# Kernel optimization log

Measured on AMD Instinct MI355X. Metric: run time of the kernel, lower is better.

Reference implementation:

```python
import jax, jax.numpy as jnp
import numpy as np
from jax import lax

B, C, H, W = 16, 128, 128, 128
C8, C16 = C // 8, C // 16
LN_EPS = 1e-5


def dct_mat(N):
    # torch_dct.dct (norm=None): X_k = 2 * sum_n x_n cos(pi*(2n+1)k/(2N))
    n = jnp.arange(N, dtype=jnp.float32)
    k = jnp.arange(N, dtype=jnp.float32)
    return 2.0 * jnp.cos(jnp.pi * (2.0 * n[None, :] + 1.0) * k[:, None] / (2.0 * N))


def setup_inputs() -> dict:
    key = jax.random.key(0)
    ks = jax.random.split(key, 20)
    s = 0.05
    return {
        "x": jax.random.normal(ks[0], (B, C, H, W), dtype=jnp.float32),
        # channel attention (1x1 convs acting on GAP -> stored as dense [out,in])
        "ca_w1": jax.random.normal(ks[1], (C8, C), dtype=jnp.float32) * s,
        "ca_b1": jnp.zeros((C8,), jnp.float32),
        "ca_w2": jax.random.normal(ks[2], (C, C8), dtype=jnp.float32) * s,
        "ca_b2": jnp.zeros((C,), jnp.float32),
        # spatial attention 9x9 conv -> 1 channel
        "sa_w": jax.random.normal(ks[3], (1, C, 9, 9), dtype=jnp.float32) * s,
        "sa_b": jnp.zeros((1,), jnp.float32),
        # frequency channel attention MLP
        "fa_w1": jax.random.normal(ks[4], (C8, C), dtype=jnp.float32) * s,
        "fa_b1": jnp.zeros((C8,), jnp.float32),
        "fa_w2": jax.random.normal(ks[5], (C, C8), dtype=jnp.float32) * s,
        "fa_b2": jnp.zeros((C,), jnp.float32),
        # global context block
        "gc_mask_w": jax.random.normal(ks[6], (C,), dtype=jnp.float32) * s,
        "gc_mask_b": jnp.zeros((), jnp.float32),
        "gc_t1_w": jax.random.normal(ks[7], (C16, C), dtype=jnp.float32) * s,
        "gc_t1_b": jnp.zeros((C16,), jnp.float32),
        "gc_ln_g": jnp.ones((C16,), jnp.float32),
        "gc_ln_b": jnp.zeros((C16,), jnp.float32),
        "gc_t2_w": jax.random.normal(ks[8], (C, C16), dtype=jnp.float32) * s,
        "gc_t2_b": jnp.zeros((C,), jnp.float32),
        # branch mixing weights + output 1x1 conv
        "alpha": jnp.ones((4,), jnp.float32),
        "out_w": jax.random.normal(ks[9], (C, C), dtype=jnp.float32) * s,
        "out_b": jnp.zeros((C,), jnp.float32),
    }


def reference(x, ca_w1, ca_b1, ca_w2, ca_b2, sa_w, sa_b,
              fa_w1, fa_b1, fa_w2, fa_b2,
              gc_mask_w, gc_mask_b, gc_t1_w, gc_t1_b, gc_ln_g, gc_ln_b,
              gc_t2_w, gc_t2_b, alpha, out_w, out_b):
    b, c, h, w = x.shape
    # --- channel attention (SE-style) ---
    gap = x.mean(axis=(2, 3))                                   # [B,C]
    hca = jax.nn.relu(gap @ ca_w1.T + ca_b1)
    ca = jax.nn.sigmoid(hca @ ca_w2.T + ca_b2)                  # [B,C]
    ac = x * ca[:, :, None, None]
    # --- spatial attention (9x9 conv -> sigmoid gate) ---
    smap = lax.conv_general_dilated(x, sa_w, (1, 1), ((4, 4), (4, 4)),
                                    dimension_numbers=("NCHW", "OIHW", "NCHW"))
    as_ = jax.nn.sigmoid(smap + sa_b[None, :, None, None]) * x
    # --- frequency channel attention (DCT-II 2d, mean over freq) ---
    Dw = dct_mat(w)
    Dh = dct_mat(h)
    xf = jnp.einsum("bchw,kw->bchk", x, Dw)
    xf = jnp.einsum("bchk,lh->bclk", xf, Dh)                    # [B,C,H,W] freq
    favg = xf.mean(axis=(2, 3))                                 # [B,C]
    hfa = jax.nn.relu(favg @ fa_w1.T + fa_b1)
    fwt = jax.nn.sigmoid(hfa @ fa_w2.T + fa_b2)
    af = x * fwt[:, :, None, None]
    # --- global context block ---
    mask = jnp.einsum("bchw,c->bhw", x, gc_mask_w) + gc_mask_b  # [B,H,W]
    mask = jax.nn.softmax(mask.reshape(b, h * w), axis=-1)      # [B,HW]
    ctx = jnp.einsum("bcp,bp->bc", x.reshape(b, c, h * w), mask)  # [B,C]
    t = ctx @ gc_t1_w.T + gc_t1_b                               # [B,C/16]
    mu = t.mean(axis=-1, keepdims=True)
    var = ((t - mu) ** 2).mean(axis=-1, keepdims=True)
    t = (t - mu) * lax.rsqrt(var + LN_EPS) * gc_ln_g + gc_ln_b
    t = jax.nn.relu(t)
    ctx2 = t @ gc_t2_w.T + gc_t2_b                              # [B,C]
    ag = x + ctx2[:, :, None, None]
    # --- softmax-weighted fusion + output 1x1 conv ---
    wts = jax.nn.softmax(alpha)
    fused = wts[0] * ac + wts[1] * as_ + wts[2] * af + wts[3] * ag
    return jnp.einsum("bchw,oc->bohw", fused, out_w) + out_b[None, :, None, None]
```

## Files before the change

kernel.cpp:

```cpp
#include <hip/hip_runtime.h>
#include <math.h>

#define B_   16
#define C_   128
#define W_   128
#define HW_  16384

#define OFF_SARR 0
#define OFF_GAP  128
#define OFF_FAVG 2176
#define OFF_CTX  4224
#define OFF_G    6272
#define OFF_CB   8320
#define OFF_WTS  10368
#define OFF_PMAX 10496
#define OFF_PSUM 10752
#define OFF_SMX  11008
#define OFF_SINV 11024
#define OFF_WT   16384
#define OFF_M    32768
#define OFF_S    (32768 + 262144)
#define OFF_SMAP (32768 + 2 * 262144)

__device__ __forceinline__ float wave_reduce_sum(float v) {
#pragma unroll
  for (int o = 32; o > 0; o >>= 1) v += __shfl_down(v, o, 64);
  return v;
}

__global__ void k0_sarr(float* __restrict__ sarr) {
  int n = threadIdx.x;
  double a = 3.14159265358979323846 * (2.0 * n + 1.0) / 256.0;
  double v = 2.0 * sin(64.0 * a) * cos(63.5 * a) / sin(0.5 * a);
  sarr[n] = (float)v;
}

__global__ __launch_bounds__(256) void k1_planered(const float* __restrict__ x,
                                                   const float* __restrict__ sarr,
                                                   float* __restrict__ gap,
                                                   float* __restrict__ favg) {
  __shared__ float sL[128];
  __shared__ float buf[8];
  int tid = threadIdx.x;
  int bc = blockIdx.x;
  if (tid < 128) sL[tid] = sarr[tid];
  __syncthreads();
  const float* xp = x + (size_t)bc * HW_;
  float s0 = 0.f, s1 = 0.f;
  for (int i = tid << 2; i < HW_; i += 1024) {
    float4 v = *(const float4*)(xp + i);
    int y = i >> 7, xs = i & 127;
    float shy = sL[y];
    float d = v.x * sL[xs] + v.y * sL[xs + 1] + v.z * sL[xs + 2] + v.w * sL[xs + 3];
    s0 += v.x + v.y + v.z + v.w;
    s1 += shy * d;
  }
  s0 = wave_reduce_sum(s0);
  s1 = wave_reduce_sum(s1);
  int lane = tid & 63, wv = tid >> 6;
  if (lane == 0) { buf[wv] = s0; buf[4 + wv] = s1; }
  __syncthreads();
  if (tid == 0) {
    gap[bc]  = (buf[0] + buf[1] + buf[2] + buf[3]) * (1.f / 16384.f);
    favg[bc] = (buf[4] + buf[5] + buf[6] + buf[7]) * (1.f / 16384.f);
  }
}

__global__ __launch_bounds__(256) void k2_masklogit(const float* __restrict__ x,
                                                    const float* __restrict__ gcw,
                                                    const float* __restrict__ gcb,
                                                    float* __restrict__ m) {
  __shared__ float gl[128];
  int tid = threadIdx.x;
  int b = blockIdx.x >> 4;
  int chunk = blockIdx.x & 15;
  if (tid < 128) gl[tid] = gcw[tid];
  __syncthreads();
  int p0 = (chunk << 10) + (tid << 2);
  const float* xp = x + (size_t)b * C_ * HW_ + p0;
  float4 acc = make_float4(0.f, 0.f, 0.f, 0.f);
  for (int c = 0; c < 128; ++c) {
    float4 v = *(const float4*)(xp + (size_t)c * HW_);
    float wv = gl[c];
    acc.x = fmaf(wv, v.x, acc.x);
    acc.y = fmaf(wv, v.y, acc.y);
    acc.z = fmaf(wv, v.z, acc.z);
    acc.w = fmaf(wv, v.w, acc.w);
  }
  float bb = gcb[0];
  acc.x += bb; acc.y += bb; acc.z += bb; acc.w += bb;
  *(float4*)(m + b * HW_ + p0) = acc;
}

__global__ __launch_bounds__(256) void k3a_part(const float* __restrict__ m,
                                                float* __restrict__ pmax,
                                                float* __restrict__ psum) {
  __shared__ float buf[8];
  int blk = blockIdx.x;
  int tid = threadIdx.x;
  float4 v = *(const float4*)(m + (blk << 10) + (tid << 2));
  float mx = fmaxf(fmaxf(v.x, v.y), fmaxf(v.z, v.w));
#pragma unroll
  for (int o = 32; o > 0; o >>= 1) mx = fmaxf(mx, __shfl_xor(mx, o, 64));
  int lane = tid & 63, wv = tid >> 6;
  if (lane == 0) buf[wv] = mx;
  __syncthreads();
  mx = fmaxf(fmaxf(buf[0], buf[1]), fmaxf(buf[2], buf[3]));
  float s = __expf(v.x - mx) + __expf(v.y - mx) + __expf(v.z - mx) + __expf(v.w - mx);
  s = wave_reduce_sum(s);
  if (lane == 0) buf[4 + wv] = s;
  __syncthreads();
  if (tid == 0) {
    pmax[blk] = mx;
    psum[blk] = buf[4] + buf[5] + buf[6] + buf[7];
  }
}

__global__ void k3b_comb(const float* __restrict__ pmax, const float* __restrict__ psum,
                         float* __restrict__ smx, float* __restrict__ sinv) {
  int tid = threadIdx.x;
  int b = tid >> 4, j = tid & 15;
  float mx = pmax[tid];
  float sm = psum[tid];
  float gmx = mx;
#pragma unroll
  for (int o = 8; o > 0; o >>= 1) gmx = fmaxf(gmx, __shfl_xor(gmx, o, 64));
  float e = sm * __expf(mx - gmx);
#pragma unroll
  for (int o = 8; o > 0; o >>= 1) e += __shfl_xor(e, o, 64);
  if (j == 0) { smx[b] = gmx; sinv[b] = 1.f / e; }
}

__global__ __launch_bounds__(256) void k3c_norm(float* __restrict__ m,
                                                const float* __restrict__ smx,
                                                const float* __restrict__ sinv) {
  int blk = blockIdx.x;
  int b = blk >> 4;
  int i = (blk << 10) + (threadIdx.x << 2);
  float mx = smx[b], inv = sinv[b];
  float4 v = *(const float4*)(m + i);
  v.x = __expf(v.x - mx) * inv;
  v.y = __expf(v.y - mx) * inv;
  v.z = __expf(v.z - mx) * inv;
  v.w = __expf(v.w - mx) * inv;
  *(float4*)(m + i) = v;
}

__global__ __launch_bounds__(256) void k4_ctx(const float* __restrict__ x,
                                              const float* __restrict__ mask,
                                              float* __restrict__ ctx) {
  __shared__ float buf[4];
  int tid = threadIdx.x;
  int bc = blockIdx.x;
  int b = bc >> 7;
  const float* xp = x + (size_t)bc * HW_;
  const float* mp = mask + b * HW_;
  float s = 0.f;
  for (int i = tid << 2; i < HW_; i += 1024) {
    float4 v = *(const float4*)(xp + i);
    float4 mk = *(const float4*)(mp + i);
    s += v.x * mk.x + v.y * mk.y + v.z * mk.z + v.w * mk.w;
  }
  s = wave_reduce_sum(s);
  if ((tid & 63) == 0) buf[tid >> 6] = s;
  __syncthreads();
  if (tid == 0) ctx[bc] = buf[0] + buf[1] + buf[2] + buf[3];
}

__global__ __launch_bounds__(128) void k5_mlp(
    const float* __restrict__ gap, const float* __restrict__ favg,
    const float* __restrict__ ctx,
    const float* __restrict__ ca_w1, const float* __restrict__ ca_b1,
    const float* __restrict__ ca_w2, const float* __restrict__ ca_b2,
    const float* __restrict__ fa_w1, const float* __restrict__ fa_b1,
    const float* __restrict__ fa_w2, const float* __restrict__ fa_b2,
    const float* __restrict__ t1w, const float* __restrict__ t1b,
    const float* __restrict__ lng, const float* __restrict__ lnb,
    const float* __restrict__ t2w, const float* __restrict__ t2b,
    const float* __restrict__ alpha,
    const float* __restrict__ out_w, const float* __restrict__ out_b,
    float* __restrict__ g, float* __restrict__ cb, float* __restrict__ wts) {
  int b = blockIdx.x, t = threadIdx.x;
  __shared__ float gapL[128], favL[128], ctxL[128], hca[16], hfa[16], tl[8], dl[128];
  gapL[t] = gap[(b << 7) + t];
  favL[t] = favg[(b << 7) + t];
  ctxL[t] = ctx[(b << 7) + t];
  __syncthreads();
  if (t < 16) {
    float a = ca_b1[t], f = fa_b1[t];
    for (int c = 0; c < 128; ++c) {
      a += gapL[c] * ca_w1[t * 128 + c];
      f += favL[c] * fa_w1[t * 128 + c];
    }
    hca[t] = fmaxf(a, 0.f);
    hfa[t] = fmaxf(f, 0.f);
  }
  if (t < 8) {
    float v = t1b[t];
    for (int c = 0; c < 128; ++c) v += ctxL[c] * t1w[t * 128 + c];
    tl[t] = v;
  }
  __syncthreads();
  float mu = 0.f;
#pragma unroll
  for (int j = 0; j < 8; ++j) mu += tl[j];
  mu *= 0.125f;
  float var = 0.f;
#pragma unroll
  for (int j = 0; j < 8; ++j) { float d = tl[j] - mu; var += d * d; }
  var *= 0.125f;
  float rs = rsqrtf(var + 1e-5f);
  float a0 = alpha[0], a1 = alpha[1], a2 = alpha[2], a3 = alpha[3];
  float am = fmaxf(fmaxf(a0, a1), fmaxf(a2, a3));
  float e0 = __expf(a0 - am), e1 = __expf(a1 - am), e2 = __expf(a2 - am), e3 = __expf(a3 - am);
  float es = 1.f / (e0 + e1 + e2 + e3);
  float w0 = e0 * es, w1 = e1 * es, w2 = e2 * es, w3 = e3 * es;
  float cav = ca_b2[t], fav = fa_b2[t], c2 = t2b[t];
#pragma unroll
  for (int j = 0; j < 16; ++j) {
    cav += hca[j] * ca_w2[t * 16 + j];
    fav += hfa[j] * fa_w2[t * 16 + j];
  }
#pragma unroll
  for (int j = 0; j < 8; ++j) {
    float tn = fmaxf((tl[j] - mu) * rs * lng[j] + lnb[j], 0.f);
    c2 += tn * t2w[t * 8 + j];
  }
  cav = 1.f / (1.f + __expf(-cav));
  fav = 1.f / (1.f + __expf(-fav));
  g[(b << 7) + t] = w0 * cav + w2 * fav + w3;
  dl[t] = w3 * c2;
  __syncthreads();
  float s = out_b[t];
  for (int c = 0; c < 128; ++c) s += out_w[t * 128 + c] * dl[c];
  cb[(b << 7) + t] = s;
  if (b == 0 && t < 4) wts[t] = (t == 0) ? w0 : (t == 1) ? w1 : (t == 2) ? w2 : w3;
}

template <int CPS>
__global__ __launch_bounds__(256) void k6_conv(const float* __restrict__ x,
                                               const float* __restrict__ saw,
                                               float* __restrict__ smap_part) {
  __shared__ float tile[40 * 136];
  int tid = threadIdx.x;
  int yt = blockIdx.x;
  int b = blockIdx.y;
  int split = blockIdx.z;
  int y0 = yt << 5;
  int rg = tid >> 5;
  int cg = tid & 31;
  int r0 = rg << 2;
  int px0 = cg << 2;
  float acc[4][4];
#pragma unroll
  for (int i = 0; i < 4; ++i)
#pragma unroll
    for (int j = 0; j < 4; ++j) acc[i][j] = 0.f;
  const float* xb = x + (size_t)b * C_ * HW_;
  int c_lo = split * CPS;

  for (int ci = 0; ci < CPS; ++ci) {
    int c = c_lo + ci;
    const float* xc = xb + (size_t)c * HW_;
    __syncthreads();
    for (int idx = tid; idx < 1360; idx += 256) {
      int row = idx / 34, c4 = idx - row * 34;
      int gy = y0 - 4 + row;
      int gx = (c4 << 2) - 4;
      float4 v = make_float4(0.f, 0.f, 0.f, 0.f);
      if (gy >= 0 && gy < 128 && gx >= 0 && gx <= 124)
        v = *(const float4*)(xc + gy * W_ + gx);
      *(float4*)(tile + row * 136 + (c4 << 2)) = v;
    }
    __syncthreads();
    const float* wrow = saw + c * 81;
#pragma unroll
    for (int ir = 0; ir < 12; ++ir) {
      const float* tp = tile + (r0 + ir) * 136 + px0;
      float4 u0 = *(const float4*)tp;
      float4 u1 = *(const float4*)(tp + 4);
      float4 u2 = *(const float4*)(tp + 8);
      float rowv[12] = {u0.x, u0.y, u0.z, u0.w, u1.x, u1.y, u1.z, u1.w,
                        u2.x, u2.y, u2.z, u2.w};
#pragma unroll
      for (int i = 0; i < 4; ++i) {
        int dy = ir - i;
        if (dy < 0 || dy > 8) continue;
#pragma unroll
        for (int dx = 0; dx < 9; ++dx) {
          float wv = wrow[dy * 9 + dx];
#pragma unroll
          for (int j = 0; j < 4; ++j)
            acc[i][j] = fmaf(wv, rowv[dx + j], acc[i][j]);
        }
      }
    }
  }
  float* op = smap_part + ((size_t)(split * B_ + b)) * HW_ + (y0 + r0) * W_ + px0;
#pragma unroll
  for (int i = 0; i < 4; ++i)
    *(float4*)(op + (size_t)i * W_) = make_float4(acc[i][0], acc[i][1], acc[i][2], acc[i][3]);
}

template <int NS>
__global__ __launch_bounds__(256) void k6b_gate(const float* __restrict__ smap_part,
                                                const float* __restrict__ wts,
                                                const float* __restrict__ sab,
                                                float* __restrict__ s) {
  int i = (blockIdx.x * 256 + threadIdx.x) << 2;
  float w1 = wts[1];
  float bb = sab[0];
  float4 a = *(const float4*)(smap_part + i);
#pragma unroll
  for (int j = 1; j < NS; ++j) {
    float4 t4 = *(const float4*)(smap_part + (size_t)j * 262144 + i);
    a.x += t4.x; a.y += t4.y; a.z += t4.z; a.w += t4.w;
  }
  float4 r;
  r.x = w1 / (1.f + __expf(-(a.x + bb)));
  r.y = w1 / (1.f + __expf(-(a.y + bb)));
  r.z = w1 / (1.f + __expf(-(a.z + bb)));
  r.w = w1 / (1.f + __expf(-(a.w + bb)));
  *(float4*)(s + i) = r;
}

__global__ __launch_bounds__(256) void k7a_transpose(const float* __restrict__ w,
                                                     float* __restrict__ wt) {
  __shared__ float t[32][33];
  int bx = blockIdx.x & 3, by = blockIdx.x >> 2;
  int lx = threadIdx.x & 31, ly = threadIdx.x >> 5;
#pragma unroll
  for (int j = 0; j < 4; ++j)
    t[ly + j * 8][lx] = w[(by * 32 + ly + j * 8) * 128 + bx * 32 + lx];
  __syncthreads();
#pragma unroll
  for (int j = 0; j < 4; ++j)
    wt[(bx * 32 + ly + j * 8) * 128 + by * 32 + lx] = t[lx][ly + j * 8];
}

__global__ __launch_bounds__(256) void k7_gemm(const float* __restrict__ x,
                                               const float* __restrict__ wt,
                                               const float* __restrict__ g,
                                               const float* __restrict__ s,
                                               const float* __restrict__ cb,
                                               float* __restrict__ out) {
  __shared__ float xm[64 * 128];
  int tid = threadIdx.x;
  int b = blockIdx.x >> 7;
  int pt = blockIdx.x & 127;
  int p0 = pt << 7;
  const float* xb = x + (size_t)b * C_ * HW_ + p0;
  const float* sb = s + b * HW_ + p0;
  int pg = tid & 15, og = tid >> 4;
  int o0 = og << 3;
  int ppA = pg << 2;
  int ppB = 64 + (pg << 2);
  float acc[8][8];
#pragma unroll
  for (int i = 0; i < 8; ++i)
#pragma unroll
    for (int j = 0; j < 8; ++j) acc[i][j] = 0.f;
  int sp4 = (tid & 31) << 2;
  int crow = tid >> 5;
  float4 sv = *(const float4*)(sb + sp4);
  for (int chunk = 0; chunk < 2; ++chunk) {
    int cbase = chunk << 6;
    __syncthreads();
#pragma unroll
    for (int pass = 0; pass < 8; ++pass) {
      int cl = (pass << 3) + crow;
      int c = cbase + cl;
      float4 v = *(const float4*)(xb + (size_t)c * HW_ + sp4);
      float gc = g[(b << 7) + c];
      float4 r;
      r.x = v.x * (gc + sv.x);
      r.y = v.y * (gc + sv.y);
      r.z = v.z * (gc + sv.z);
      r.w = v.w * (gc + sv.w);
      *(float4*)(xm + (cl << 7) + sp4) = r;
    }
    __syncthreads();
#pragma unroll 4
    for (int cl = 0; cl < 64; ++cl) {
      const float* wp = wt + ((size_t)(cbase + cl) << 7) + o0;
      float4 wa = *(const float4*)wp;
      float4 wb = *(const float4*)(wp + 4);
      const float* xrow = xm + (cl << 7);
      float4 xa = *(const float4*)(xrow + ppA);
      float4 xb4 = *(const float4*)(xrow + ppB);
      float wv[8] = {wa.x, wa.y, wa.z, wa.w, wb.x, wb.y, wb.z, wb.w};
      float xv[8] = {xa.x, xa.y, xa.z, xa.w, xb4.x, xb4.y, xb4.z, xb4.w};
#pragma unroll
      for (int i = 0; i < 8; ++i)
#pragma unroll
        for (int j = 0; j < 8; ++j) acc[i][j] = fmaf(wv[i], xv[j], acc[i][j]);
    }
  }
  size_t obase = ((size_t)((b << 7) + o0)) * HW_ + p0;
#pragma unroll
  for (int i = 0; i < 8; ++i) {
    float cv = cb[(b << 7) + o0 + i];
    float4 r0 = make_float4(acc[i][0] + cv, acc[i][1] + cv, acc[i][2] + cv, acc[i][3] + cv);
    float4 r1 = make_float4(acc[i][4] + cv, acc[i][5] + cv, acc[i][6] + cv, acc[i][7] + cv);
    *(float4*)(out + obase + (size_t)i * HW_ + ppA) = r0;
    *(float4*)(out + obase + (size_t)i * HW_ + ppB) = r1;
  }
}

extern "C" void kernel_launch(void* const* d_in, const int* in_sizes, int n_in,
                              void* d_out, int out_size, void* d_ws, size_t ws_size,
                              hipStream_t stream) {
  const float* x       = (const float*)d_in[0];
  const float* ca_w1   = (const float*)d_in[1];
  const float* ca_b1   = (const float*)d_in[2];
  const float* ca_w2   = (const float*)d_in[3];
  const float* ca_b2   = (const float*)d_in[4];
  const float* sa_w    = (const float*)d_in[5];
  const float* sa_b    = (const float*)d_in[6];
  const float* fa_w1   = (const float*)d_in[7];
  const float* fa_b1   = (const float*)d_in[8];
  const float* fa_w2   = (const float*)d_in[9];
  const float* fa_b2   = (const float*)d_in[10];
  const float* gc_mw   = (const float*)d_in[11];
  const float* gc_mb   = (const float*)d_in[12];
  const float* gc_t1w  = (const float*)d_in[13];
  const float* gc_t1b  = (const float*)d_in[14];
  const float* gc_lng  = (const float*)d_in[15];
  const float* gc_lnb  = (const float*)d_in[16];
  const float* gc_t2w  = (const float*)d_in[17];
  const float* gc_t2b  = (const float*)d_in[18];
  const float* alpha   = (const float*)d_in[19];
  const float* out_w   = (const float*)d_in[20];
  const float* out_b   = (const float*)d_in[21];
  float* out = (float*)d_out;
  float* ws = (float*)d_ws;

  float* sarr = ws + OFF_SARR;
  float* gap  = ws + OFF_GAP;
  float* favg = ws + OFF_FAVG;
  float* ctx  = ws + OFF_CTX;
  float* g    = ws + OFF_G;
  float* cb   = ws + OFF_CB;
  float* wts  = ws + OFF_WTS;
  float* pmax = ws + OFF_PMAX;
  float* psum = ws + OFF_PSUM;
  float* smx  = ws + OFF_SMX;
  float* sinv = ws + OFF_SINV;
  float* wt   = ws + OFF_WT;
  float* m    = ws + OFF_M;
  float* s    = ws + OFF_S;
  float* smap = ws + OFF_SMAP;

  size_t need16 = (size_t)(OFF_SMAP + 16 * 262144) * sizeof(float);
  size_t need8  = (size_t)(OFF_SMAP + 8 * 262144) * sizeof(float);

  k0_sarr<<<1, 128, 0, stream>>>(sarr);
  k1_planered<<<2048, 256, 0, stream>>>(x, sarr, gap, favg);
  k2_masklogit<<<256, 256, 0, stream>>>(x, gc_mw, gc_mb, m);
  k3a_part<<<256, 256, 0, stream>>>(m, pmax, psum);
  k3b_comb<<<1, 256, 0, stream>>>(pmax, psum, smx, sinv);
  k3c_norm<<<256, 256, 0, stream>>>(m, smx, sinv);
  k4_ctx<<<2048, 256, 0, stream>>>(x, m, ctx);
  k5_mlp<<<16, 128, 0, stream>>>(gap, favg, ctx, ca_w1, ca_b1, ca_w2, ca_b2,
                                 fa_w1, fa_b1, fa_w2, fa_b2, gc_t1w, gc_t1b,
                                 gc_lng, gc_lnb, gc_t2w, gc_t2b, alpha,
                                 out_w, out_b, g, cb, wts);
  k7a_transpose<<<16, 256, 0, stream>>>(out_w, wt);
  if (ws_size >= need16) {
    k6_conv<8><<<dim3(4, 16, 16), 256, 0, stream>>>(x, sa_w, smap);
    k6b_gate<16><<<256, 256, 0, stream>>>(smap, wts, sa_b, s);
  } else if (ws_size >= need8) {
    k6_conv<16><<<dim3(4, 16, 8), 256, 0, stream>>>(x, sa_w, smap);
    k6b_gate<8><<<256, 256, 0, stream>>>(smap, wts, sa_b, s);
  } else {
    k6_conv<32><<<dim3(4, 16, 4), 256, 0, stream>>>(x, sa_w, smap);
    k6b_gate<4><<<256, 256, 0, stream>>>(smap, wts, sa_b, s);
  }
  k7_gemm<<<2048, 256, 0, stream>>>(x, wt, g, s, cb, out);
}
```

Measured before the change: 532.1 us.

## Fuse reduction kernels and move output GEMM to split-bf16 MFMA

Merges the plane-reduction and mask-logit passes into one launch, folds the softmax combine/normalize into the context kernel, computes DCT sums analytically in-kernel, and folds the transpose into the MLP kernel as a bf16 hi/lo weight split. The spatial conv gains register prefetching of the next channel tile and a finer split, and the gate sigmoid moves into the GEMM. The 1x1 output GEMM now runs on 32x32x16 bf16 MFMA with three-term hi/lo splitting to approximate fp32 accuracy. This cuts launches and extra passes over intermediate buffers but adds in-loop bf16 conversion work and slightly different rounding.

```diff
diff --git a/kernel.cpp b/kernel.cpp
--- a/kernel.cpp
+++ b/kernel.cpp
@@ -6,168 +6,154 @@
 #define W_   128
 #define HW_  16384
 
-#define OFF_SARR 0
-#define OFF_GAP  128
-#define OFF_FAVG 2176
-#define OFF_CTX  4224
-#define OFF_G    6272
-#define OFF_CB   8320
-#define OFF_WTS  10368
-#define OFF_PMAX 10496
-#define OFF_PSUM 10752
-#define OFF_SMX  11008
-#define OFF_SINV 11024
-#define OFF_WT   16384
-#define OFF_M    32768
-#define OFF_S    (32768 + 262144)
-#define OFF_SMAP (32768 + 2 * 262144)
+typedef unsigned short ushort_t;
+typedef unsigned int uint_t;
+typedef short sh4 __attribute__((ext_vector_type(4)));
+typedef short short8 __attribute__((ext_vector_type(8)));
+typedef float f32x16 __attribute__((ext_vector_type(16)));
+
+#define OFF_GAP   0
+#define OFF_FAVG  2048
+#define OFF_CTX   4096
+#define OFF_G     6144
+#define OFF_CB    8192
+#define OFF_WTS   10240
+#define OFF_PMAX  10496
+#define OFF_PSUM  12544
+#define OFF_WHI   16384
+#define OFF_WLO   24576
+#define OFF_M     32768
+#define OFF_SMAP  294912
 
 __device__ __forceinline__ float wave_reduce_sum(float v) {
 #pragma unroll
-  for (int o = 32; o > 0; o >>= 1) v += __shfl_down(v, o, 64);
+  for (int o = 32; o > 0; o >>= 1) v += __shfl_xor(v, o, 64);
   return v;
 }
-
-__global__ void k0_sarr(float* __restrict__ sarr) {
-  int n = threadIdx.x;
-  double a = 3.14159265358979323846 * (2.0 * n + 1.0) / 256.0;
-  double v = 2.0 * sin(64.0 * a) * cos(63.5 * a) / sin(0.5 * a);
-  sarr[n] = (float)v;
-}
-
-__global__ __launch_bounds__(256) void k1_planered(const float* __restrict__ x,
-                                                   const float* __restrict__ sarr,
-                                                   float* __restrict__ gap,
-                                                   float* __restrict__ favg) {
-  __shared__ float sL[128];
-  __shared__ float buf[8];
-  int tid = threadIdx.x;
-  int bc = blockIdx.x;
-  if (tid < 128) sL[tid] = sarr[tid];
-  __syncthreads();
-  const float* xp = x + (size_t)bc * HW_;
-  float s0 = 0.f, s1 = 0.f;
-  for (int i = tid << 2; i < HW_; i += 1024) {
-    float4 v = *(const float4*)(xp + i);
-    int y = i >> 7, xs = i & 127;
-    float shy = sL[y];
-    float d = v.x * sL[xs] + v.y * sL[xs + 1] + v.z * sL[xs + 2] + v.w * sL[xs + 3];
-    s0 += v.x + v.y + v.z + v.w;
-    s1 += shy * d;
-  }
-  s0 = wave_reduce_sum(s0);
-  s1 = wave_reduce_sum(s1);
-  int lane = tid & 63, wv = tid >> 6;
-  if (lane == 0) { buf[wv] = s0; buf[4 + wv] = s1; }
-  __syncthreads();
-  if (tid == 0) {
-    gap[bc]  = (buf[0] + buf[1] + buf[2] + buf[3]) * (1.f / 16384.f);
-    favg[bc] = (buf[4] + buf[5] + buf[6] + buf[7]) * (1.f / 16384.f);
-  }
-}
-
-__global__ __launch_bounds__(256) void k2_masklogit(const float* __restrict__ x,
-                                                    const float* __restrict__ gcw,
-                                                    const float* __restrict__ gcb,
-                                                    float* __restrict__ m) {
-  __shared__ float gl[128];
-  int tid = threadIdx.x;
-  int b = blockIdx.x >> 4;
-  int chunk = blockIdx.x & 15;
-  if (tid < 128) gl[tid] = gcw[tid];
-  __syncthreads();
-  int p0 = (chunk << 10) + (tid << 2);
-  const float* xp = x + (size_t)b * C_ * HW_ + p0;
-  float4 acc = make_float4(0.f, 0.f, 0.f, 0.f);
-  for (int c = 0; c < 128; ++c) {
-    float4 v = *(const float4*)(xp + (size_t)c * HW_);
-    float wv = gl[c];
-    acc.x = fmaf(wv, v.x, acc.x);
-    acc.y = fmaf(wv, v.y, acc.y);
-    acc.z = fmaf(wv, v.z, acc.z);
-    acc.w = fmaf(wv, v.w, acc.w);
-  }
-  float bb = gcb[0];
-  acc.x += bb; acc.y += bb; acc.z += bb; acc.w += bb;
-  *(float4*)(m + b * HW_ + p0) = acc;
-}
-
-__global__ __launch_bounds__(256) void k3a_part(const float* __restrict__ m,
+__device__ __forceinline__ float wave_reduce_max(float v) {
+#pragma unroll
+  for (int o = 32; o > 0; o >>= 1) v = fmaxf(v, __shfl_xor(v, o, 64));
+  return v;
+}
+__device__ __forceinline__ ushort_t rne_bf16(float f) {
+  uint_t u = __float_as_uint(f);
+  return (ushort_t)((u + 0x7FFFu + ((u >> 16) & 1u)) >> 16);
+}
+__device__ __forceinline__ float bf16_to_f(ushort_t h) {
+  return __uint_as_float(((uint_t)h) << 16);
+}
+
+__global__ __launch_bounds__(256) void n1_stats(const float* __restrict__ x,
+                                                const float* __restrict__ gcw,
+                                                const float* __restrict__ gcb,
+                                                float* __restrict__ gap,
+                                                float* __restrict__ favg,
+                                                float* __restrict__ m,
                                                 float* __restrict__ pmax,
                                                 float* __restrict__ psum) {
-  __shared__ float buf[8];
-  int blk = blockIdx.x;
   int tid = threadIdx.x;
-  float4 v = *(const float4*)(m + (blk << 10) + (tid << 2));
-  float mx = fmaxf(fmaxf(v.x, v.y), fmaxf(v.z, v.w));
-#pragma unroll
-  for (int o = 32; o > 0; o >>= 1) mx = fmaxf(mx, __shfl_xor(mx, o, 64));
-  int lane = tid & 63, wv = tid >> 6;
-  if (lane == 0) buf[wv] = mx;
-  __syncthreads();
-  mx = fmaxf(fmaxf(buf[0], buf[1]), fmaxf(buf[2], buf[3]));
-  float s = __expf(v.x - mx) + __expf(v.y - mx) + __expf(v.z - mx) + __expf(v.w - mx);
-  s = wave_reduce_sum(s);
-  if (lane == 0) buf[4 + wv] = s;
-  __syncthreads();
-  if (tid == 0) {
-    pmax[blk] = mx;
-    psum[blk] = buf[4] + buf[5] + buf[6] + buf[7];
-  }
-}
-
-__global__ void k3b_comb(const float* __restrict__ pmax, const float* __restrict__ psum,
-                         float* __restrict__ smx, float* __restrict__ sinv) {
-  int tid = threadIdx.x;
-  int b = tid >> 4, j = tid & 15;
-  float mx = pmax[tid];
-  float sm = psum[tid];
-  float gmx = mx;
-#pragma unroll
-  for (int o = 8; o > 0; o >>= 1) gmx = fmaxf(gmx, __shfl_xor(gmx, o, 64));
-  float e = sm * __expf(mx - gmx);
-#pragma unroll
-  for (int o = 8; o > 0; o >>= 1) e += __shfl_xor(e, o, 64);
-  if (j == 0) { smx[b] = gmx; sinv[b] = 1.f / e; }
-}
-
-__global__ __launch_bounds__(256) void k3c_norm(float* __restrict__ m,
-                                                const float* __restrict__ smx,
-                                                const float* __restrict__ sinv) {
-  int blk = blockIdx.x;
-  int b = blk >> 4;
-  int i = (blk << 10) + (threadIdx.x << 2);
-  float mx = smx[b], inv = sinv[b];
-  float4 v = *(const float4*)(m + i);
-  v.x = __expf(v.x - mx) * inv;
-  v.y = __expf(v.y - mx) * inv;
-  v.z = __expf(v.z - mx) * inv;
-  v.w = __expf(v.w - mx) * inv;
-  *(float4*)(m + i) = v;
-}
-
-__global__ __launch_bounds__(256) void k4_ctx(const float* __restrict__ x,
-                                              const float* __restrict__ mask,
+  if (blockIdx.x < 2048) {
+    __shared__ float sL[128];
+    __shared__ float buf[8];
+    int bc = blockIdx.x;
+    if (tid < 128) {
+      float a2 = 0.006135923151542565f * (float)(2 * tid + 1);
+      float ct = __cosf(a2) / __sinf(a2);
+      sL[tid] = 1.f + ((tid & 1) ? -ct : ct);
+    }
+    __syncthreads();
+    const float* xp = x + (size_t)bc * HW_;
+    float s0 = 0.f, s1 = 0.f;
+    for (int i = tid << 2; i < HW_; i += 1024) {
+      float4 v = *(const float4*)(xp + i);
+      int y = i >> 7, xs = i & 127;
+      float shy = sL[y];
+      float d = v.x * sL[xs] + v.y * sL[xs + 1] + v.z * sL[xs + 2] + v.w * sL[xs + 3];
+      s0 += v.x + v.y + v.z + v.w;
+      s1 += shy * d;
+    }
+    s0 = wave_reduce_sum(s0);
+    s1 = wave_reduce_sum(s1);
+    int lane = tid & 63, wv = tid >> 6;
+    if (lane == 0) { buf[wv] = s0; buf[4 + wv] = s1; }
+    __syncthreads();
+    if (tid == 0) {
+      gap[bc]  = (buf[0] + buf[1] + buf[2] + buf[3]) * (1.f / 16384.f);
+      favg[bc] = (buf[4] + buf[5] + buf[6] + buf[7]) * (1.f / 16384.f);
+    }
+  } else {
+    __shared__ float macc[256];
+    __shared__ float bmax[4], bsum[4];
+    int blk = blockIdx.x - 2048;
+    int b = blk >> 7, pc = blk & 127;
+    int p0 = pc << 7;
+    int pl = tid & 127, chalf = tid >> 7;
+    const float* xp = x + ((size_t)b * C_ + (size_t)chalf * 64) * HW_ + p0 + pl;
+    const float* gw = gcw + chalf * 64;
+    float acc = 0.f;
+#pragma unroll 8
+    for (int i = 0; i < 64; ++i) acc = fmaf(gw[i], xp[(size_t)i * HW_], acc);
+    macc[tid] = acc;
+    __syncthreads();
+    float mval = 0.f;
+    bool act = tid < 128;
+    if (act) {
+      mval = macc[tid] + macc[tid + 128] + gcb[0];
+      m[(size_t)b * HW_ + p0 + tid] = mval;
+    }
+    float mx = act ? mval : -1e30f;
+    mx = wave_reduce_max(mx);
+    if ((tid & 63) == 0) bmax[tid >> 6] = mx;
+    __syncthreads();
+    float gmax = fmaxf(bmax[0], bmax[1]);
+    float se = act ? __expf(mval - gmax) : 0.f;
+    se = wave_reduce_sum(se);
+    if ((tid & 63) == 0) bsum[tid >> 6] = se;
+    __syncthreads();
+    if (tid == 0) { pmax[blk] = gmax; psum[blk] = bsum[0] + bsum[1]; }
+  }
+}
+
+__global__ __launch_bounds__(256) void n2_ctx(const float* __restrict__ x,
+                                              const float* __restrict__ m,
+                                              const float* __restrict__ pmax,
+                                              const float* __restrict__ psum,
                                               float* __restrict__ ctx) {
+  __shared__ float sred[8];
   __shared__ float buf[4];
+  __shared__ float sm_sh, si_sh;
   int tid = threadIdx.x;
   int bc = blockIdx.x;
   int b = bc >> 7;
+  float pm = -1e30f, ps = 0.f;
+  if (tid < 128) { pm = pmax[(b << 7) + tid]; ps = psum[(b << 7) + tid]; }
+  float gm = wave_reduce_max(pm);
+  if ((tid & 63) == 0) sred[tid >> 6] = gm;
+  __syncthreads();
+  gm = fmaxf(sred[0], sred[1]);
+  float e = (tid < 128) ? ps * __expf(pm - gm) : 0.f;
+  e = wave_reduce_sum(e);
+  if ((tid & 63) == 0) sred[4 + (tid >> 6)] = e;
+  __syncthreads();
+  if (tid == 0) { sm_sh = gm; si_sh = 1.f / (sred[4] + sred[5]); }
+  __syncthreads();
+  float smx = sm_sh, sinv = si_sh;
   const float* xp = x + (size_t)bc * HW_;
-  const float* mp = mask + b * HW_;
+  const float* mp = m + (size_t)b * HW_;
   float s = 0.f;
   for (int i = tid << 2; i < HW_; i += 1024) {
     float4 v = *(const float4*)(xp + i);
-    float4 mk = *(const float4*)(mp + i);
-    s += v.x * mk.x + v.y * mk.y + v.z * mk.z + v.w * mk.w;
+    float4 mv = *(const float4*)(mp + i);
+    s += v.x * __expf(mv.x - smx) + v.y * __expf(mv.y - smx) +
+         v.z * __expf(mv.z - smx) + v.w * __expf(mv.w - smx);
   }
   s = wave_reduce_sum(s);
   if ((tid & 63) == 0) buf[tid >> 6] = s;
   __syncthreads();
-  if (tid == 0) ctx[bc] = buf[0] + buf[1] + buf[2] + buf[3];
-}
-
-__global__ __launch_bounds__(128) void k5_mlp(
+  if (tid == 0) ctx[bc] = (buf[0] + buf[1] + buf[2] + buf[3]) * sinv;
+}
+
+__global__ __launch_bounds__(128) void n3_mlp(
     const float* __restrict__ gap, const float* __restrict__ favg,
     const float* __restrict__ ctx,
     const float* __restrict__ ca_w1, const float* __restrict__ ca_b1,
@@ -179,8 +165,22 @@
     const float* __restrict__ t2w, const float* __restrict__ t2b,
     const float* __restrict__ alpha,
     const float* __restrict__ out_w, const float* __restrict__ out_b,
-    float* __restrict__ g, float* __restrict__ cb, float* __restrict__ wts) {
-  int b = blockIdx.x, t = threadIdx.x;
+    float* __restrict__ g, float* __restrict__ cb, float* __restrict__ wts,
+    ushort_t* __restrict__ whi, ushort_t* __restrict__ wlo) {
+  int t = threadIdx.x;
+  if (blockIdx.x >= 16) {
+    int base = (blockIdx.x - 16) * 1024 + t;
+#pragma unroll
+    for (int k = 0; k < 8; ++k) {
+      int idx = base + k * 128;
+      float w = out_w[idx];
+      ushort_t h = rne_bf16(w);
+      whi[idx] = h;
+      wlo[idx] = rne_bf16(w - bf16_to_f(h));
+    }
+    return;
+  }
+  int b = blockIdx.x;
   __shared__ float gapL[128], favL[128], ctxL[128], hca[16], hfa[16], tl[8], dl[128];
   gapL[t] = gap[(b << 7) + t];
   favL[t] = favg[(b << 7) + t];
@@ -238,7 +238,7 @@
 }
 
 template <int CPS>
-__global__ __launch_bounds__(256) void k6_conv(const float* __restrict__ x,
+__global__ __launch_bounds__(256) void n4_conv(const float* __restrict__ x,
                                                const float* __restrict__ saw,
                                                float* __restrict__ smap_part) {
   __shared__ float tile[40 * 136];
@@ -259,21 +259,41 @@
   const float* xb = x + (size_t)b * C_ * HW_;
   int c_lo = split * CPS;
 
+  float4 pre[6];
+  auto issue_loads = [&](int c) {
+    const float* xc = xb + (size_t)c * HW_;
+#pragma unroll
+    for (int k = 0; k < 6; ++k) {
+      int idx = tid + (k << 8);
+      if (idx < 1360) {
+        int row = idx / 34, c4 = idx - row * 34;
+        int gy = y0 - 4 + row;
+        int gx = (c4 << 2) - 4;
+        float4 v = make_float4(0.f, 0.f, 0.f, 0.f);
+        if (gy >= 0 && gy < 128 && gx >= 0 && gx <= 124)
+          v = *(const float4*)(xc + gy * W_ + gx);
+        pre[k] = v;
+      }
+    }
+  };
+  auto write_tile = [&]() {
+#pragma unroll
+    for (int k = 0; k < 6; ++k) {
+      int idx = tid + (k << 8);
+      if (idx < 1360) {
+        int row = idx / 34, c4 = idx - row * 34;
+        *(float4*)(tile + row * 136 + (c4 << 2)) = pre[k];
+      }
+    }
+  };
+
+  issue_loads(c_lo);
   for (int ci = 0; ci < CPS; ++ci) {
-    int c = c_lo + ci;
-    const float* xc = xb + (size_t)c * HW_;
-    __syncthreads();
-    for (int idx = tid; idx < 1360; idx += 256) {
-      int row = idx / 34, c4 = idx - row * 34;
-      int gy = y0 - 4 + row;
-      int gx = (c4 << 2) - 4;
-      float4 v = make_float4(0.f, 0.f, 0.f, 0.f);
-      if (gy >= 0 && gy < 128 && gx >= 0 && gx <= 124)
-        v = *(const float4*)(xc + gy * W_ + gx);
-      *(float4*)(tile + row * 136 + (c4 << 2)) = v;
-    }
-    __syncthreads();
-    const float* wrow = saw + c * 81;
+    __syncthreads();
+    write_tile();
+    __syncthreads();
+    if (ci + 1 < CPS) issue_loads(c_lo + ci + 1);
+    const float* wrow = saw + (c_lo + ci) * 81;
 #pragma unroll
     for (int ir = 0; ir < 12; ++ir) {
       const float* tp = tile + (r0 + ir) * 136 + px0;
@@ -302,109 +322,130 @@
     *(float4*)(op + (size_t)i * W_) = make_float4(acc[i][0], acc[i][1], acc[i][2], acc[i][3]);
 }
 
-template <int NS>
-__global__ __launch_bounds__(256) void k6b_gate(const float* __restrict__ smap_part,
-                                                const float* __restrict__ wts,
-                                                const float* __restrict__ sab,
-                                                float* __restrict__ s) {
-  int i = (blockIdx.x * 256 + threadIdx.x) << 2;
-  float w1 = wts[1];
-  float bb = sab[0];
-  float4 a = *(const float4*)(smap_part + i);
-#pragma unroll
-  for (int j = 1; j < NS; ++j) {
-    float4 t4 = *(const float4*)(smap_part + (size_t)j * 262144 + i);
-    a.x += t4.x; a.y += t4.y; a.z += t4.z; a.w += t4.w;
-  }
-  float4 r;
-  r.x = w1 / (1.f + __expf(-(a.x + bb)));
-  r.y = w1 / (1.f + __expf(-(a.y + bb)));
-  r.z = w1 / (1.f + __expf(-(a.z + bb)));
-  r.w = w1 / (1.f + __expf(-(a.w + bb)));
-  *(float4*)(s + i) = r;
-}
-
-__global__ __launch_bounds__(256) void k7a_transpose(const float* __restrict__ w,
-                                                     float* __restrict__ wt) {
-  __shared__ float t[32][33];
-  int bx = blockIdx.x & 3, by = blockIdx.x >> 2;
-  int lx = threadIdx.x & 31, ly = threadIdx.x >> 5;
-#pragma unroll
-  for (int j = 0; j < 4; ++j)
-    t[ly + j * 8][lx] = w[(by * 32 + ly + j * 8) * 128 + bx * 32 + lx];
-  __syncthreads();
-#pragma unroll
-  for (int j = 0; j < 4; ++j)
-    wt[(bx * 32 + ly + j * 8) * 128 + by * 32 + lx] = t[lx][ly + j * 8];
-}
-
-__global__ __launch_bounds__(256) void k7_gemm(const float* __restrict__ x,
-                                               const float* __restrict__ wt,
+__global__ __launch_bounds__(256) void n5_gemm(const float* __restrict__ x,
+                                               const ushort_t* __restrict__ whi,
+                                               const ushort_t* __restrict__ wlo,
                                                const float* __restrict__ g,
-                                               const float* __restrict__ s,
+                                               const float* __restrict__ smap,
+                                               const float* __restrict__ wts,
+                                               const float* __restrict__ sab,
                                                const float* __restrict__ cb,
-                                               float* __restrict__ out) {
-  __shared__ float xm[64 * 128];
+                                               float* __restrict__ out,
+                                               int ns) {
+  __shared__ float xm[64 * 132];
+  __shared__ float s_lds[128], g_lds[128], cb_lds[128];
   int tid = threadIdx.x;
   int b = blockIdx.x >> 7;
   int pt = blockIdx.x & 127;
   int p0 = pt << 7;
-  const float* xb = x + (size_t)b * C_ * HW_ + p0;
-  const float* sb = s + b * HW_ + p0;
-  int pg = tid & 15, og = tid >> 4;
-  int o0 = og << 3;
-  int ppA = pg << 2;
-  int ppB = 64 + (pg << 2);
-  float acc[8][8];
-#pragma unroll
-  for (int i = 0; i < 8; ++i)
-#pragma unroll
-    for (int j = 0; j < 8; ++j) acc[i][j] = 0.f;
-  int sp4 = (tid & 31) << 2;
-  int crow = tid >> 5;
-  float4 sv = *(const float4*)(sb + sp4);
+
+  if (tid < 128) {
+    float a = sab[0];
+    const float* sp = smap + (size_t)b * HW_ + p0 + tid;
+    for (int j = 0; j < ns; ++j) a += sp[(size_t)j * (B_ * HW_)];
+    s_lds[tid] = wts[1] / (1.f + __expf(-a));
+  } else {
+    int t2 = tid - 128;
+    g_lds[t2] = g[(b << 7) + t2];
+    cb_lds[t2] = cb[(b << 7) + t2];
+  }
+
+  int l = tid & 63;
+  int w = tid >> 6;
+  int wr = w >> 1, wc = w & 1;
+  int h = l >> 5;
+  int ln31 = l & 31;
+  int c_l = tid >> 2, pq = tid & 3;
+
+  f32x16 acc00, acc01, acc10, acc11;
+#pragma unroll
+  for (int j = 0; j < 16; ++j) { acc00[j] = 0.f; acc01[j] = 0.f; acc10[j] = 0.f; acc11[j] = 0.f; }
+
   for (int chunk = 0; chunk < 2; ++chunk) {
-    int cbase = chunk << 6;
-    __syncthreads();
-#pragma unroll
-    for (int pass = 0; pass < 8; ++pass) {
-      int cl = (pass << 3) + crow;
-      int c = cbase + cl;
-      float4 v = *(const float4*)(xb + (size_t)c * HW_ + sp4);
-      float gc = g[(b << 7) + c];
+    __syncthreads();
+    float gc = g_lds[(chunk << 6) + c_l];
+    const float* xg = x + ((size_t)b * C_ + (chunk << 6) + c_l) * HW_ + p0 + (pq << 5);
+    float* wl = xm + c_l * 132 + (pq << 5);
+#pragma unroll
+    for (int i = 0; i < 8; ++i) {
+      float4 v = *(const float4*)(xg + (i << 2));
+      float4 sv = *(const float4*)(s_lds + (pq << 5) + (i << 2));
       float4 r;
       r.x = v.x * (gc + sv.x);
       r.y = v.y * (gc + sv.y);
       r.z = v.z * (gc + sv.z);
       r.w = v.w * (gc + sv.w);
-      *(float4*)(xm + (cl << 7) + sp4) = r;
-    }
-    __syncthreads();
-#pragma unroll 4
-    for (int cl = 0; cl < 64; ++cl) {
-      const float* wp = wt + ((size_t)(cbase + cl) << 7) + o0;
-      float4 wa = *(const float4*)wp;
-      float4 wb = *(const float4*)(wp + 4);
-      const float* xrow = xm + (cl << 7);
-      float4 xa = *(const float4*)(xrow + ppA);
-      float4 xb4 = *(const float4*)(xrow + ppB);
-      float wv[8] = {wa.x, wa.y, wa.z, wa.w, wb.x, wb.y, wb.z, wb.w};
-      float xv[8] = {xa.x, xa.y, xa.z, xa.w, xb4.x, xb4.y, xb4.z, xb4.w};
-#pragma unroll
-      for (int i = 0; i < 8; ++i)
-#pragma unroll
-        for (int j = 0; j < 8; ++j) acc[i][j] = fmaf(wv[i], xv[j], acc[i][j]);
-    }
-  }
-  size_t obase = ((size_t)((b << 7) + o0)) * HW_ + p0;
-#pragma unroll
-  for (int i = 0; i < 8; ++i) {
-    float cv = cb[(b << 7) + o0 + i];
-    float4 r0 = make_float4(acc[i][0] + cv, acc[i][1] + cv, acc[i][2] + cv, acc[i][3] + cv);
-    float4 r1 = make_float4(acc[i][4] + cv, acc[i][5] + cv, acc[i][6] + cv, acc[i][7] + cv);
-    *(float4*)(out + obase + (size_t)i * HW_ + ppA) = r0;
-    *(float4*)(out + obase + (size_t)i * HW_ + ppB) = r1;
-  }
+      *(float4*)(wl + (i << 2)) = r;
+    }
+    __syncthreads();
+#pragma unroll
+    for (int ks = 0; ks < 4; ++ks) {
+      int cb16 = ks << 4;
+      short8 ahi0, ahi1, alo0, alo1;
+      {
+        int cg0 = (chunk << 6) + cb16 + (h << 2);
+        const ushort_t* wp0 = whi + ((wr << 6) + ln31) * 128 + cg0;
+        const ushort_t* wp1 = whi + ((wr << 6) + 32 + ln31) * 128 + cg0;
+        const ushort_t* vp0 = wlo + ((wr << 6) + ln31) * 128 + cg0;
+        const ushort_t* vp1 = wlo + ((wr << 6) + 32 + ln31) * 128 + cg0;
+        sh4 a0 = *(const sh4*)(const void*)wp0, a1 = *(const sh4*)(const void*)(wp0 + 8);
+        ahi0 = __builtin_shufflevector(a0, a1, 0, 1, 2, 3, 4, 5, 6, 7);
+        sh4 b0 = *(const sh4*)(const void*)wp1, b1 = *(const sh4*)(const void*)(wp1 + 8);
+        ahi1 = __builtin_shufflevector(b0, b1, 0, 1, 2, 3, 4, 5, 6, 7);
+        sh4 c0 = *(const sh4*)(const void*)vp0, c1 = *(const sh4*)(const void*)(vp0 + 8);
+        alo0 = __builtin_shufflevector(c0, c1, 0, 1, 2, 3, 4, 5, 6, 7);
+        sh4 d0 = *(const sh4*)(const void*)vp1, d1 = *(const sh4*)(const void*)(vp1 + 8);
+        alo1 = __builtin_shufflevector(d0, d1, 0, 1, 2, 3, 4, 5, 6, 7);
+      }
+#pragma unroll
+      for (int ptile = 0; ptile < 2; ++ptile) {
+        int pcol = (wc << 6) + (ptile << 5) + ln31;
+        short8 bhi, blo;
+#pragma unroll
+        for (int j = 0; j < 8; ++j) {
+          int co = (j & 3) + ((j >> 2) << 3) + (h << 2);
+          float f = xm[(cb16 + co) * 132 + pcol];
+          uint_t u = __float_as_uint(f);
+          uint_t hu = (u + 0x7FFFu + ((u >> 16) & 1u)) >> 16;
+          float lof = f - __uint_as_float(hu << 16);
+          uint_t ul = __float_as_uint(lof);
+          uint_t lu = (ul + 0x7FFFu + ((ul >> 16) & 1u)) >> 16;
+          bhi[j] = (short)hu;
+          blo[j] = (short)lu;
+        }
+        if (ptile == 0) {
+          acc00 = __builtin_amdgcn_mfma_f32_32x32x16_bf16(ahi0, bhi, acc00, 0, 0, 0);
+          acc00 = __builtin_amdgcn_mfma_f32_32x32x16_bf16(ahi0, blo, acc00, 0, 0, 0);
+          acc00 = __builtin_amdgcn_mfma_f32_32x32x16_bf16(alo0, bhi, acc00, 0, 0, 0);
+          acc10 = __builtin_amdgcn_mfma_f32_32x32x16_bf16(ahi1, bhi, acc10, 0, 0, 0);
+          acc10 = __builtin_amdgcn_mfma_f32_32x32x16_bf16(ahi1, blo, acc10, 0, 0, 0);
+          acc10 = __builtin_amdgcn_mfma_f32_32x32x16_bf16(alo1, bhi, acc10, 0, 0, 0);
+        } else {
+          acc01 = __builtin_amdgcn_mfma_f32_32x32x16_bf16(ahi0, bhi, acc01, 0, 0, 0);
+          acc01 = __builtin_amdgcn_mfma_f32_32x32x16_bf16(ahi0, blo, acc01, 0, 0, 0);
+          acc01 = __builtin_amdgcn_mfma_f32_32x32x16_bf16(alo0, bhi, acc01, 0, 0, 0);
+          acc11 = __builtin_amdgcn_mfma_f32_32x32x16_bf16(ahi1, bhi, acc11, 0, 0, 0);
+          acc11 = __builtin_amdgcn_mfma_f32_32x32x16_bf16(ahi1, blo, acc11, 0, 0, 0);
+          acc11 = __builtin_amdgcn_mfma_f32_32x32x16_bf16(alo1, bhi, acc11, 0, 0, 0);
+        }
+      }
+    }
+  }
+  size_t ob = (size_t)(b << 7) * HW_ + p0;
+#define STORE_FRAG(ACC, OT, PT)                                                  \
+  {                                                                              \
+    int obase = (wr << 6) + ((OT) << 5);                                         \
+    int pp = (wc << 6) + ((PT) << 5) + ln31;                                     \
+    _Pragma("unroll") for (int reg = 0; reg < 16; ++reg) {                       \
+      int o = obase + (reg & 3) + ((reg >> 2) << 3) + (h << 2);                  \
+      out[ob + (size_t)o * HW_ + pp] = (ACC)[reg] + cb_lds[o];                   \
+    }                                                                            \
+  }
+  STORE_FRAG(acc00, 0, 0)
+  STORE_FRAG(acc10, 1, 0)
+  STORE_FRAG(acc01, 0, 1)
+  STORE_FRAG(acc11, 1, 1)
+#undef STORE_FRAG
 }
 
 extern "C" void kernel_launch(void* const* d_in, const int* in_sizes, int n_in,
@@ -435,7 +476,6 @@
   float* out = (float*)d_out;
   float* ws = (float*)d_ws;
 
-  float* sarr = ws + OFF_SARR;
   float* gap  = ws + OFF_GAP;
   float* favg = ws + OFF_FAVG;
   float* ctx  = ws + OFF_CTX;
@@ -444,37 +484,28 @@
   float* wts  = ws + OFF_WTS;
   float* pmax = ws + OFF_PMAX;
   float* psum = ws + OFF_PSUM;
-  float* smx  = ws + OFF_SMX;
-  float* sinv = ws + OFF_SINV;
-  float* wt   = ws + OFF_WT;
+  ushort_t* whi = (ushort_t*)(ws + OFF_WHI);
+  ushort_t* wlo = (ushort_t*)(ws + OFF_WLO);
   float* m    = ws + OFF_M;
-  float* s    = ws + OFF_S;
   float* smap = ws + OFF_SMAP;
 
-  size_t need16 = (size_t)(OFF_SMAP + 16 * 262144) * sizeof(float);
-  size_t need8  = (size_t)(OFF_SMAP + 8 * 262144) * sizeof(float);
-
-  k0_sarr<<<1, 128, 0, stream>>>(sarr);
-  k1_planered<<<2048, 256, 0, stream>>>(x, sarr, gap, favg);
-  k2_masklogit<<<256, 256, 0, stream>>>(x, gc_mw, gc_mb, m);
-  k3a_part<<<256, 256, 0, stream>>>(m, pmax, psum);
-  k3b_comb<<<1, 256, 0, stream>>>(pmax, psum, smx, sinv);
-  k3c_norm<<<256, 256, 0, stream>>>(m, smx, sinv);
-  k4_ctx<<<2048, 256, 0, stream>>>(x, m, ctx);
-  k5_mlp<<<16, 128, 0, stream>>>(gap, favg, ctx, ca_w1, ca_b1, ca_w2, ca_b2,
+  auto need = [](int ns) { return (size_t)(OFF_SMAP + (size_t)ns * 262144) * sizeof(float); };
+
+  n1_stats<<<4096, 256, 0, stream>>>(x, gc_mw, gc_mb, gap, favg, m, pmax, psum);
+  n2_ctx<<<2048, 256, 0, stream>>>(x, m, pmax, psum, ctx);
+  n3_mlp<<<32, 128, 0, stream>>>(gap, favg, ctx, ca_w1, ca_b1, ca_w2, ca_b2,
                                  fa_w1, fa_b1, fa_w2, fa_b2, gc_t1w, gc_t1b,
                                  gc_lng, gc_lnb, gc_t2w, gc_t2b, alpha,
-                                 out_w, out_b, g, cb, wts);
-  k7a_transpose<<<16, 256, 0, stream>>>(out_w, wt);
-  if (ws_size >= need16) {
-    k6_conv<8><<<dim3(4, 16, 16), 256, 0, stream>>>(x, sa_w, smap);
-    k6b_gate<16><<<256, 256, 0, stream>>>(smap, wts, sa_b, s);
-  } else if (ws_size >= need8) {
-    k6_conv<16><<<dim3(4, 16, 8), 256, 0, stream>>>(x, sa_w, smap);
-    k6b_gate<8><<<256, 256, 0, stream>>>(smap, wts, sa_b, s);
+                                 out_w, out_b, g, cb, wts, whi, wlo);
+  int ns;
+  if (ws_size >= need(32)) {
+    ns = 32; n4_conv<4><<<dim3(4, 16, 32), 256, 0, stream>>>(x, sa_w, smap);
+  } else if (ws_size >= need(16)) {
+    ns = 16; n4_conv<8><<<dim3(4, 16, 16), 256, 0, stream>>>(x, sa_w, smap);
+  } else if (ws_size >= need(8)) {
+    ns = 8; n4_conv<16><<<dim3(4, 16, 8), 256, 0, stream>>>(x, sa_w, smap);
   } else {
-    k6_conv<32><<<dim3(4, 16, 4), 256, 0, stream>>>(x, sa_w, smap);
-    k6b_gate<4><<<256, 256, 0, stream>>>(smap, wts, sa_b, s);
-  }
-  k7_gemm<<<2048, 256, 0, stream>>>(x, wt, g, s, cb, out);
-}
+    ns = 4; n4_conv<32><<<dim3(4, 16, 4), 256, 0, stream>>>(x, sa_w, smap);
+  }
+  n5_gemm<<<2048, 256, 0, stream>>>(x, whi, wlo, g, smap, wts, sa_b, cb, out, ns);
+}
```

New measurement: 553.4 us. 4.0% more time.
